# Performance work log

Hardware: AMD Instinct MI355X
Metric: run time of the kernel (lower is better)

Reference implementation:

```python
import jax, jax.numpy as jnp
import numpy as np

N, T, D, M = 16, 4096, 256, 512


def setup_inputs() -> dict:
    key = jax.random.key(0)
    k1, k2 = jax.random.split(key)
    x = jax.random.normal(k1, (N, T, D), dtype=jnp.float32)
    # codebook initialized like the module: uniform(-1/M, 1/M) then row-normalized
    init_bound = 1.0 / M
    emb = jax.random.uniform(k2, (M, D), dtype=jnp.float32, minval=-init_bound, maxval=init_bound)
    emb = emb / (jnp.linalg.norm(emb, axis=1, keepdims=True) + 1e-4)
    return {"x": x, "embedding": emb}


def reference(x, embedding):
    sg = jax.lax.stop_gradient
    # L2_distance: distances computed against the row-normalized codebook,
    # but the gather uses the raw (unnormalized) codebook.
    emb_norm = embedding / (jnp.linalg.norm(embedding, axis=1, keepdims=True) + 1e-4)
    x_flat = sg(x).reshape(-1, D)  # (N*T, D), detached in torch
    distances = (jnp.sum(emb_norm ** 2, axis=1)[None, :]
                 + jnp.sum(x_flat ** 2, axis=1, keepdims=True)
                 - 2.0 * (x_flat @ emb_norm.T))  # (N*T, M)
    indices = jnp.argmin(distances, axis=-1)  # (N*T,)
    encodings = jax.nn.one_hot(indices, M, dtype=jnp.float32)  # (N*T, M)
    quantized = embedding[indices].reshape(x.shape)  # (N, T, D)

    commitment_loss = jnp.mean((sg(x) - quantized) ** 2)
    quantized_ = x + sg(quantized - x)           # straight-through
    quantized_ = (quantized_ + quantized) / 2.0  # averaged with raw-grad path

    avg_probs = jnp.mean(encodings, axis=0)  # (M,)
    perplexity = jnp.exp(-jnp.sum(avg_probs * jnp.log(avg_probs + 1e-10)))
    return quantized_, commitment_loss, perplexity
```

## Files before the change

kernel.cpp:

```cpp
#include <hip/hip_runtime.h>
#include <hip/hip_bf16.h>


typedef _Float16 half8_t __attribute__((ext_vector_type(8)));
typedef _Float16 half4_t __attribute__((ext_vector_type(4)));
typedef float f32x4 __attribute__((ext_vector_type(4)));

static constexpr int kRows = 65536;
static constexpr int kD = 256;
static constexpr int kM = 512;
static constexpr int kBM = 64;

typedef const unsigned int __attribute__((address_space(1)))* gas_t;
typedef unsigned int __attribute__((address_space(3)))* las_t;

__global__ void vq_prep(const float* __restrict__ emb, _Float16* __restrict__ swz,
                        float* __restrict__ bias, unsigned int* __restrict__ hist,
                        float* __restrict__ loss) {
    const int j = blockIdx.x;
    const int lane = threadIdx.x;
    float4 v = ((const float4*)(emb + j * kD))[lane];
    float ss = v.x * v.x + v.y * v.y + v.z * v.z + v.w * v.w;
    #pragma unroll
    for (int off = 32; off > 0; off >>= 1) ss += __shfl_xor(ss, off);
    const float scale = 1.0f / (sqrtf(ss) + 1e-4f);
    if (lane == 0) bias[j] = 0.5f * ss * scale * scale;
    half4_t h;
    h[0] = (_Float16)(v.x * scale);
    h[1] = (_Float16)(v.y * scale);
    h[2] = (_Float16)(v.z * scale);
    h[3] = (_Float16)(v.w * scale);
    const int k0 = lane * 4;
    const int ko = k0 >> 5;
    const int qd = (k0 >> 3) & 3;
    const int jj = k0 & 7;
    const int off_h = (j >> 4) * 4096 + ko * 512 + (qd * 16 + (j & 15)) * 8 + jj;
    *(half4_t*)(swz + off_h) = h;
    if (j == 0) {
        for (int b = lane; b < kM; b += 64) hist[b] = 0u;
        if (lane == 0) loss[0] = 0.0f;
    }
}

__global__ __launch_bounds__(512, 8) void vq_main(
    const float* __restrict__ x, const float* __restrict__ emb,
    const _Float16* __restrict__ bswz, const float* __restrict__ bias,
    unsigned int* __restrict__ hist, float* __restrict__ loss_accum,
    float* __restrict__ out) {
    __shared__ _Float16 bb0[32 * kD];
    __shared__ _Float16 bb1[32 * kD];
    __shared__ float lbias[kM];
    __shared__ unsigned int lhist[kM];
    __shared__ int lidx[kBM];
    __shared__ float lbv[kBM * 2];
    __shared__ int lbi[kBM * 2];
    __shared__ float lred[8];

    const int t = threadIdx.x;
    const int row0 = blockIdx.x * kBM;
    const int wave = t >> 6;
    const int lane = t & 63;
    const int qd = lane >> 4;
    const int ln = lane & 15;
    const int m0 = (wave & 3) * 16;
    const int h = wave >> 2;

    lhist[t] = 0u;
    lbias[t] = bias[t];

    {
        const _Float16* src = bswz + t * 8;
        __builtin_amdgcn_global_load_lds((gas_t)(const void*)(src),
                                         (las_t)(void*)(bb0 + t * 8), 16, 0, 0);
        __builtin_amdgcn_global_load_lds((gas_t)(const void*)(src + 4096),
                                         (las_t)(void*)(bb0 + t * 8 + 4096), 16, 0, 0);
    }

    half8_t a[8];
    {
        const float* xr = x + (size_t)(row0 + m0 + ln) * kD + qd * 8;
        #pragma unroll
        for (int ko = 0; ko < 8; ++ko) {
            const float4 v0 = *(const float4*)(xr + ko * 32);
            const float4 v1 = *(const float4*)(xr + ko * 32 + 4);
            half8_t hh;
            hh[0] = (_Float16)v0.x; hh[1] = (_Float16)v0.y;
            hh[2] = (_Float16)v0.z; hh[3] = (_Float16)v0.w;
            hh[4] = (_Float16)v1.x; hh[5] = (_Float16)v1.y;
            hh[6] = (_Float16)v1.z; hh[7] = (_Float16)v1.w;
            a[ko] = hh;
        }
    }
    __syncthreads();

    float bv[4] = {-1e30f, -1e30f, -1e30f, -1e30f};
    int bi[4] = {0, 0, 0, 0};

    auto issue = [&](int s, _Float16* dst) {
        const _Float16* src = bswz + (size_t)s * 8192 + t * 8;
        __builtin_amdgcn_global_load_lds((gas_t)(const void*)(src),
                                         (las_t)(void*)(dst + t * 8), 16, 0, 0);
        __builtin_amdgcn_global_load_lds((gas_t)(const void*)(src + 4096),
                                         (las_t)(void*)(dst + t * 8 + 4096), 16, 0, 0);
    };
    auto compute = [&](int s, const _Float16* buf) {
        const int c = s * 32 + h * 16 + ln;
        const float bbias = lbias[c];
        f32x4 acc = {-bbias, -bbias, -bbias, -bbias};
        const half8_t* bp = (const half8_t*)buf + h * 512 + lane;
        #pragma unroll
        for (int ko = 0; ko < 8; ++ko)
            acc = __builtin_amdgcn_mfma_f32_16x16x32_f16(a[ko], bp[ko * 64], acc, 0, 0, 0);
        #pragma unroll
        for (int r = 0; r < 4; ++r)
            if (acc[r] > bv[r] || (acc[r] == bv[r] && c < bi[r])) { bv[r] = acc[r]; bi[r] = c; }
    };

    #pragma unroll 1
    for (int s = 0; s < 16; s += 2) {
        issue(s + 1, bb1);
        compute(s, bb0);
        __syncthreads();
        if (s + 2 < 16) issue(s + 2, bb0);
        compute(s + 1, bb1);
        __syncthreads();
    }

    #pragma unroll
    for (int r = 0; r < 4; ++r) {
        #pragma unroll
        for (int off = 1; off < 16; off <<= 1) {
            const float ov = __shfl_xor(bv[r], off);
            const int oi = __shfl_xor(bi[r], off);
            if (ov > bv[r] || (ov == bv[r] && oi < bi[r])) { bv[r] = ov; bi[r] = oi; }
        }
        if (ln == 0) {
            const int row = m0 + qd * 4 + r;
            lbv[row * 2 + h] = bv[r];
            lbi[row * 2 + h] = bi[r];
        }
    }
    __syncthreads();
    if (t < kBM) {
        const float v0 = lbv[t * 2], v1 = lbv[t * 2 + 1];
        const int i0 = lbi[t * 2], i1 = lbi[t * 2 + 1];
        const int win = (v1 > v0 || (v1 == v0 && i1 < i0)) ? i1 : i0;
        lidx[t] = win;
        atomicAdd(&lhist[win], 1u);
    }
    __syncthreads();

    float lsum = 0.0f;
    {
        const float* xg = x + (size_t)row0 * kD;
        float* og = out + (size_t)row0 * kD;
        #pragma unroll
        for (int i = 0; i < 8; ++i) {
            const int g = t * 4 + i * 2048;
            const int r = g >> 8;
            const float4 xv = *(const float4*)(xg + g);
            const int idx = lidx[r];
            const float4 q = *(const float4*)(emb + (size_t)idx * kD + (g & 255));
            const float d0 = xv.x - q.x, d1 = xv.y - q.y, d2 = xv.z - q.z, d3 = xv.w - q.w;
            lsum += d0 * d0 + d1 * d1 + d2 * d2 + d3 * d3;
            float4 o;
            o.x = ((xv.x + (q.x - xv.x)) + q.x) * 0.5f;
            o.y = ((xv.y + (q.y - xv.y)) + q.y) * 0.5f;
            o.z = ((xv.z + (q.z - xv.z)) + q.z) * 0.5f;
            o.w = ((xv.w + (q.w - xv.w)) + q.w) * 0.5f;
            *(float4*)&og[g] = o;
        }
    }
    #pragma unroll
    for (int off = 32; off > 0; off >>= 1) lsum += __shfl_xor(lsum, off);
    if (lane == 0) lred[wave] = lsum;
    __syncthreads();
    if (t == 0) {
        float bs = 0.f;
        #pragma unroll
        for (int w = 0; w < 8; ++w) bs += lred[w];
        atomicAdd(loss_accum, bs);
    }

    const unsigned int h0 = lhist[t];
    if (h0) atomicAdd(&hist[t], h0);
}

__global__ void vq_final(const unsigned int* __restrict__ hist,
                         const float* __restrict__ loss_accum,
                         float* __restrict__ out) {
    const int t = threadIdx.x;
    __shared__ float sr[4];
    float s = 0.0f;
    for (int b = t; b < kM; b += 256) {
        const float p = (float)hist[b] * (1.0f / 65536.0f);
        s += p * logf(p + 1e-10f);
    }
    #pragma unroll
    for (int off = 32; off > 0; off >>= 1) s += __shfl_xor(s, off);
    if ((t & 63) == 0) sr[t >> 6] = s;
    __syncthreads();
    if (t == 0) {
        const float tot = sr[0] + sr[1] + sr[2] + sr[3];
        out[16777217] = expf(-tot);
        out[16777216] = loss_accum[0] * (1.0f / 16777216.0f);
    }
}

extern "C" void kernel_launch(void* const* d_in, const int* in_sizes, int n_in,
                              void* d_out, int out_size, void* d_ws, size_t ws_size,
                              hipStream_t stream) {
    const float* x = (const float*)d_in[0];
    const float* emb = (const float*)d_in[1];
    char* ws = (char*)d_ws;
    _Float16* bswz = (_Float16*)ws;
    float* bias = (float*)(ws + 262144);
    unsigned int* hist = (unsigned int*)(ws + 262144 + 2048);
    float* loss = (float*)(ws + 262144 + 4096);
    float* out = (float*)d_out;

    vq_prep<<<kM, 64, 0, stream>>>(emb, bswz, bias, hist, loss);
    vq_main<<<kRows / kBM, 512, 0, stream>>>(x, emb, bswz, bias, hist, loss, out);
    vq_final<<<1, 256, 0, stream>>>(hist, loss, out);
}
```

Baseline: 144.9 us.

## Compute commitment loss from matmul scores and write codebook rows directly

```diff
diff --git a/kernel.cpp b/kernel.cpp
--- a/kernel.cpp
+++ b/kernel.cpp
@@ -1,5 +1,4 @@
 #include <hip/hip_runtime.h>
-#include <hip/hip_bf16.h>
 
 
 typedef _Float16 half8_t __attribute__((ext_vector_type(8)));
@@ -15,16 +14,21 @@
 typedef unsigned int __attribute__((address_space(3)))* las_t;
 
 __global__ void vq_prep(const float* __restrict__ emb, _Float16* __restrict__ swz,
-                        float* __restrict__ bias, unsigned int* __restrict__ hist,
-                        float* __restrict__ loss) {
+                        float* __restrict__ bias, float2* __restrict__ cab,
+                        unsigned int* __restrict__ hist, float* __restrict__ loss) {
     const int j = blockIdx.x;
     const int lane = threadIdx.x;
     float4 v = ((const float4*)(emb + j * kD))[lane];
     float ss = v.x * v.x + v.y * v.y + v.z * v.z + v.w * v.w;
     #pragma unroll
     for (int off = 32; off > 0; off >>= 1) ss += __shfl_xor(ss, off);
-    const float scale = 1.0f / (sqrtf(ss) + 1e-4f);
-    if (lane == 0) bias[j] = 0.5f * ss * scale * scale;
+    const float s = sqrtf(ss) + 1e-4f;
+    const float scale = 1.0f / s;
+    if (lane == 0) {
+        bias[j] = 0.5f * ss * scale * scale;
+        cab[j] = make_float2(ss * (1.0f - scale),
+                             -2.0f * s);
+    }
     half4_t h;
     h[0] = (_Float16)(v.x * scale);
     h[1] = (_Float16)(v.y * scale);
@@ -42,28 +46,28 @@
     }
 }
 
-__global__ __launch_bounds__(512, 8) void vq_main(
+__global__ __launch_bounds__(512, 4) void vq_main(
     const float* __restrict__ x, const float* __restrict__ emb,
     const _Float16* __restrict__ bswz, const float* __restrict__ bias,
-    unsigned int* __restrict__ hist, float* __restrict__ loss_accum,
-    float* __restrict__ out) {
+    const float2* __restrict__ cab, unsigned int* __restrict__ hist,
+    float* __restrict__ loss_accum, float* __restrict__ out) {
     __shared__ _Float16 bb0[32 * kD];
     __shared__ _Float16 bb1[32 * kD];
     __shared__ float lbias[kM];
     __shared__ unsigned int lhist[kM];
-    __shared__ int lidx[kBM];
-    __shared__ float lbv[kBM * 2];
-    __shared__ int lbi[kBM * 2];
-    __shared__ float lred[8];
+    __shared__ float lbv[kBM][2];
+    __shared__ int   lbi[kBM][2];
+    __shared__ float lssq[kBM];
+    __shared__ int   lidx[kBM];
 
     const int t = threadIdx.x;
-    const int row0 = blockIdx.x * kBM;
     const int wave = t >> 6;
     const int lane = t & 63;
     const int qd = lane >> 4;
     const int ln = lane & 15;
     const int m0 = (wave & 3) * 16;
     const int h = wave >> 2;
+    const int row0 = blockIdx.x * kBM;
 
     lhist[t] = 0u;
     lbias[t] = bias[t];
@@ -77,6 +81,7 @@
     }
 
     half8_t a[8];
+    float ssq = 0.0f;
     {
         const float* xr = x + (size_t)(row0 + m0 + ln) * kD + qd * 8;
         #pragma unroll
@@ -89,8 +94,14 @@
             hh[4] = (_Float16)v1.x; hh[5] = (_Float16)v1.y;
             hh[6] = (_Float16)v1.z; hh[7] = (_Float16)v1.w;
             a[ko] = hh;
-        }
-    }
+            ssq += v0.x*v0.x + v0.y*v0.y + v0.z*v0.z + v0.w*v0.w
+                 + v1.x*v1.x + v1.y*v1.y + v1.z*v1.z + v1.w*v1.w;
+        }
+    }
+    ssq += __shfl_xor(ssq, 16);
+    ssq += __shfl_xor(ssq, 32);
+    if (h == 0 && qd == 0) lssq[m0 + ln] = ssq;
+
     __syncthreads();
 
     float bv[4] = {-1e30f, -1e30f, -1e30f, -1e30f};
@@ -136,54 +147,43 @@
         }
         if (ln == 0) {
             const int row = m0 + qd * 4 + r;
-            lbv[row * 2 + h] = bv[r];
-            lbi[row * 2 + h] = bi[r];
-        }
-    }
-    __syncthreads();
+            lbv[row][h] = bv[r];
+            lbi[row][h] = bi[r];
+        }
+    }
+    __syncthreads();
+
+    float term = 0.0f;
     if (t < kBM) {
-        const float v0 = lbv[t * 2], v1 = lbv[t * 2 + 1];
-        const int i0 = lbi[t * 2], i1 = lbi[t * 2 + 1];
-        const int win = (v1 > v0 || (v1 == v0 && i1 < i0)) ? i1 : i0;
+        const float v0 = lbv[t][0], v1 = lbv[t][1];
+        const int i0 = lbi[t][0], i1 = lbi[t][1];
+        const bool take1 = (v1 > v0);
+        const int win = take1 ? i1 : i0;
+        const float sc = take1 ? v1 : v0;
         lidx[t] = win;
         atomicAdd(&lhist[win], 1u);
-    }
-    __syncthreads();
-
-    float lsum = 0.0f;
+        const float2 cc = cab[win];
+        term = lssq[t] + cc.x + cc.y * sc;
+    }
+    if (wave == 0) {
+        #pragma unroll
+        for (int off = 32; off > 0; off >>= 1) term += __shfl_xor(term, off);
+        if (lane == 0) atomicAdd(loss_accum, term);
+    }
+    __syncthreads();
+
     {
-        const float* xg = x + (size_t)row0 * kD;
-        float* og = out + (size_t)row0 * kD;
-        #pragma unroll
+        float* og = out + (size_t)(row0 + wave * 8) * kD;
+        #pragma unroll 4
         for (int i = 0; i < 8; ++i) {
-            const int g = t * 4 + i * 2048;
-            const int r = g >> 8;
-            const float4 xv = *(const float4*)(xg + g);
-            const int idx = lidx[r];
-            const float4 q = *(const float4*)(emb + (size_t)idx * kD + (g & 255));
-            const float d0 = xv.x - q.x, d1 = xv.y - q.y, d2 = xv.z - q.z, d3 = xv.w - q.w;
-            lsum += d0 * d0 + d1 * d1 + d2 * d2 + d3 * d3;
-            float4 o;
-            o.x = ((xv.x + (q.x - xv.x)) + q.x) * 0.5f;
-            o.y = ((xv.y + (q.y - xv.y)) + q.y) * 0.5f;
-            o.z = ((xv.z + (q.z - xv.z)) + q.z) * 0.5f;
-            o.w = ((xv.w + (q.w - xv.w)) + q.w) * 0.5f;
-            *(float4*)&og[g] = o;
-        }
-    }
-    #pragma unroll
-    for (int off = 32; off > 0; off >>= 1) lsum += __shfl_xor(lsum, off);
-    if (lane == 0) lred[wave] = lsum;
-    __syncthreads();
-    if (t == 0) {
-        float bs = 0.f;
-        #pragma unroll
-        for (int w = 0; w < 8; ++w) bs += lred[w];
-        atomicAdd(loss_accum, bs);
-    }
-
-    const unsigned int h0 = lhist[t];
-    if (h0) atomicAdd(&hist[t], h0);
+            const int idx = lidx[wave * 8 + i];
+            const float4 q = *(const float4*)(emb + (size_t)idx * kD + lane * 4);
+            *(float4*)(og + i * kD + lane * 4) = q;
+        }
+    }
+
+    const unsigned int hv = lhist[t];
+    if (hv) atomicAdd(&hist[t], hv);
 }
 
 __global__ void vq_final(const unsigned int* __restrict__ hist,
@@ -215,11 +215,12 @@
     char* ws = (char*)d_ws;
     _Float16* bswz = (_Float16*)ws;
     float* bias = (float*)(ws + 262144);
-    unsigned int* hist = (unsigned int*)(ws + 262144 + 2048);
-    float* loss = (float*)(ws + 262144 + 4096);
+    unsigned int* hist = (unsigned int*)(ws + 264192);
+    float* loss = (float*)(ws + 266240);
+    float2* cab = (float2*)(ws + 266256);
     float* out = (float*)d_out;
 
-    vq_prep<<<kM, 64, 0, stream>>>(emb, bswz, bias, hist, loss);
-    vq_main<<<kRows / kBM, 512, 0, stream>>>(x, emb, bswz, bias, hist, loss, out);
+    vq_prep<<<kM, 64, 0, stream>>>(emb, bswz, bias, cab, hist, loss);
+    vq_main<<<kRows / kBM, 512, 0, stream>>>(x, emb, bswz, bias, cab, hist, loss, out);
     vq_final<<<1, 256, 0, stream>>>(hist, loss, out);
 }
```

After: 182.9 us. +26.2%, slower.

## Fuse prep, main and final kernels into one cooperative launch

Applied to the files above, without the earlier changes.

```diff
diff --git a/kernel.cpp b/kernel.cpp
--- a/kernel.cpp
+++ b/kernel.cpp
@@ -1,5 +1,7 @@
 #include <hip/hip_runtime.h>
-#include <hip/hip_bf16.h>
+#include <hip/hip_cooperative_groups.h>
+
+namespace cg = cooperative_groups;
 
 
 typedef _Float16 half8_t __attribute__((ext_vector_type(8)));
@@ -13,6 +15,214 @@
 
 typedef const unsigned int __attribute__((address_space(1)))* gas_t;
 typedef unsigned int __attribute__((address_space(3)))* las_t;
+
+__device__ __forceinline__ void vq_main_body(
+    const int blk,
+    const float* __restrict__ x, const float* __restrict__ emb,
+    const _Float16* __restrict__ bswz, const float* __restrict__ bias,
+    unsigned int* __restrict__ hist, float* __restrict__ loss_accum,
+    float* __restrict__ out) {
+    __shared__ _Float16 bb0[32 * kD];
+    __shared__ _Float16 bb1[32 * kD];
+    __shared__ float lbias[kM];
+    __shared__ unsigned int lhist[kM];
+    __shared__ int lidx[kBM];
+    __shared__ float lbv[kBM * 2];
+    __shared__ int lbi[kBM * 2];
+    __shared__ float lred[8];
+
+    const int t = threadIdx.x;
+    const int wave = t >> 6;
+    const int lane = t & 63;
+    const int qd = lane >> 4;
+    const int ln = lane & 15;
+    const int m0 = (wave & 3) * 16;
+    const int h = wave >> 2;
+    const int row0 = blk * kBM;
+
+    lhist[t] = 0u;
+    lbias[t] = bias[t];
+
+    {
+        const _Float16* src = bswz + t * 8;
+        __builtin_amdgcn_global_load_lds((gas_t)(const void*)(src),
+                                         (las_t)(void*)(bb0 + t * 8), 16, 0, 0);
+        __builtin_amdgcn_global_load_lds((gas_t)(const void*)(src + 4096),
+                                         (las_t)(void*)(bb0 + t * 8 + 4096), 16, 0, 0);
+    }
+
+    half8_t a[8];
+    {
+        const float* xr = x + (size_t)(row0 + m0 + ln) * kD + qd * 8;
+        #pragma unroll
+        for (int ko = 0; ko < 8; ++ko) {
+            const float4 v0 = *(const float4*)(xr + ko * 32);
+            const float4 v1 = *(const float4*)(xr + ko * 32 + 4);
+            half8_t hh;
+            hh[0] = (_Float16)v0.x; hh[1] = (_Float16)v0.y;
+            hh[2] = (_Float16)v0.z; hh[3] = (_Float16)v0.w;
+            hh[4] = (_Float16)v1.x; hh[5] = (_Float16)v1.y;
+            hh[6] = (_Float16)v1.z; hh[7] = (_Float16)v1.w;
+            a[ko] = hh;
+        }
+    }
+    __syncthreads();
+
+    float bv[4] = {-1e30f, -1e30f, -1e30f, -1e30f};
+    int bi[4] = {0, 0, 0, 0};
+
+    auto issue = [&](int s, _Float16* dst) {
+        const _Float16* src = bswz + (size_t)s * 8192 + t * 8;
+        __builtin_amdgcn_global_load_lds((gas_t)(const void*)(src),
+                                         (las_t)(void*)(dst + t * 8), 16, 0, 0);
+        __builtin_amdgcn_global_load_lds((gas_t)(const void*)(src + 4096),
+                                         (las_t)(void*)(dst + t * 8 + 4096), 16, 0, 0);
+    };
+    auto compute = [&](int s, const _Float16* buf) {
+        const int c = s * 32 + h * 16 + ln;
+        const float bbias = lbias[c];
+        f32x4 acc = {-bbias, -bbias, -bbias, -bbias};
+        const half8_t* bp = (const half8_t*)buf + h * 512 + lane;
+        #pragma unroll
+        for (int ko = 0; ko < 8; ++ko)
+            acc = __builtin_amdgcn_mfma_f32_16x16x32_f16(a[ko], bp[ko * 64], acc, 0, 0, 0);
+        #pragma unroll
+        for (int r = 0; r < 4; ++r)
+            if (acc[r] > bv[r] || (acc[r] == bv[r] && c < bi[r])) { bv[r] = acc[r]; bi[r] = c; }
+    };
+
+    #pragma unroll 1
+    for (int s = 0; s < 16; s += 2) {
+        issue(s + 1, bb1);
+        compute(s, bb0);
+        __syncthreads();
+        if (s + 2 < 16) issue(s + 2, bb0);
+        compute(s + 1, bb1);
+        __syncthreads();
+    }
+
+    #pragma unroll
+    for (int r = 0; r < 4; ++r) {
+        #pragma unroll
+        for (int off = 1; off < 16; off <<= 1) {
+            const float ov = __shfl_xor(bv[r], off);
+            const int oi = __shfl_xor(bi[r], off);
+            if (ov > bv[r] || (ov == bv[r] && oi < bi[r])) { bv[r] = ov; bi[r] = oi; }
+        }
+        if (ln == 0) {
+            const int row = m0 + qd * 4 + r;
+            lbv[row * 2 + h] = bv[r];
+            lbi[row * 2 + h] = bi[r];
+        }
+    }
+    __syncthreads();
+    if (t < kBM) {
+        const float v0 = lbv[t * 2], v1 = lbv[t * 2 + 1];
+        const int i0 = lbi[t * 2], i1 = lbi[t * 2 + 1];
+        const int win = (v1 > v0 || (v1 == v0 && i1 < i0)) ? i1 : i0;
+        lidx[t] = win;
+        atomicAdd(&lhist[win], 1u);
+    }
+    __syncthreads();
+
+    float lsum = 0.0f;
+    {
+        const float* xg = x + (size_t)row0 * kD;
+        float* og = out + (size_t)row0 * kD;
+        #pragma unroll
+        for (int i = 0; i < 8; ++i) {
+            const int g = t * 4 + i * 2048;
+            const int r = g >> 8;
+            const float4 xv = *(const float4*)(xg + g);
+            const int idx = lidx[r];
+            const float4 q = *(const float4*)(emb + (size_t)idx * kD + (g & 255));
+            const float d0 = xv.x - q.x, d1 = xv.y - q.y, d2 = xv.z - q.z, d3 = xv.w - q.w;
+            lsum += d0 * d0 + d1 * d1 + d2 * d2 + d3 * d3;
+            float4 o;
+            o.x = ((xv.x + (q.x - xv.x)) + q.x) * 0.5f;
+            o.y = ((xv.y + (q.y - xv.y)) + q.y) * 0.5f;
+            o.z = ((xv.z + (q.z - xv.z)) + q.z) * 0.5f;
+            o.w = ((xv.w + (q.w - xv.w)) + q.w) * 0.5f;
+            *(float4*)&og[g] = o;
+        }
+    }
+    #pragma unroll
+    for (int off = 32; off > 0; off >>= 1) lsum += __shfl_xor(lsum, off);
+    if (lane == 0) lred[wave] = lsum;
+    __syncthreads();
+    if (t == 0) {
+        float bs = 0.f;
+        #pragma unroll
+        for (int w = 0; w < 8; ++w) bs += lred[w];
+        atomicAdd(loss_accum, bs);
+    }
+
+    const unsigned int h0 = lhist[t];
+    if (h0) atomicAdd(&hist[t], h0);
+}
+
+__global__ __launch_bounds__(512, 8) void vq_fused(
+    const float* __restrict__ x, const float* __restrict__ emb,
+    _Float16* __restrict__ bswz, float* __restrict__ bias,
+    unsigned int* __restrict__ hist, float* __restrict__ loss_accum,
+    unsigned int* __restrict__ cnt, float* __restrict__ out) {
+    __shared__ float fred[8];
+    __shared__ unsigned int lrank;
+
+    const int t = threadIdx.x;
+    const int wave = t >> 6;
+    const int lane = t & 63;
+    const int blk = blockIdx.x;
+
+    if (blk < 64) {
+        const int j = blk * 8 + wave;
+        float4 v = ((const float4*)(emb + j * kD))[lane];
+        float ss = v.x * v.x + v.y * v.y + v.z * v.z + v.w * v.w;
+        #pragma unroll
+        for (int off = 32; off > 0; off >>= 1) ss += __shfl_xor(ss, off);
+        const float scale = 1.0f / (sqrtf(ss) + 1e-4f);
+        if (lane == 0) bias[j] = 0.5f * ss * scale * scale;
+        half4_t hh;
+        hh[0] = (_Float16)(v.x * scale);
+        hh[1] = (_Float16)(v.y * scale);
+        hh[2] = (_Float16)(v.z * scale);
+        hh[3] = (_Float16)(v.w * scale);
+        const int k0 = lane * 4;
+        const int ko = k0 >> 5;
+        const int qdp = (k0 >> 3) & 3;
+        const int jj = k0 & 7;
+        const int off_h = (j >> 4) * 4096 + ko * 512 + (qdp * 16 + (j & 15)) * 8 + jj;
+        *(half4_t*)(bswz + off_h) = hh;
+    } else if (blk == 64) {
+        atomicExch(&hist[t], 0u);
+        if (t == 0) { atomicExch(loss_accum, 0.0f); atomicExch(cnt, 0u); }
+    }
+    cg::this_grid().sync();
+
+    vq_main_body(blk, x, emb, bswz, bias, hist, loss_accum, out);
+
+    asm volatile("s_waitcnt vmcnt(0)" ::: "memory");
+    __syncthreads();
+    if (t == 0) lrank = atomicAdd(cnt, 1u);
+    __syncthreads();
+    if (lrank == (unsigned int)(gridDim.x - 1)) {
+        const unsigned int hv = atomicAdd(&hist[t], 0u);
+        const float p = (float)hv * (1.0f / 65536.0f);
+        float s = p * logf(p + 1e-10f);
+        #pragma unroll
+        for (int off = 32; off > 0; off >>= 1) s += __shfl_xor(s, off);
+        if (lane == 0) fred[wave] = s;
+        __syncthreads();
+        if (t == 0) {
+            float tot = 0.0f;
+            #pragma unroll
+            for (int w = 0; w < 8; ++w) tot += fred[w];
+            const float lt = atomicAdd(loss_accum, 0.0f);
+            out[16777217] = expf(-tot);
+            out[16777216] = lt * (1.0f / 16777216.0f);
+        }
+    }
+}
 
 __global__ void vq_prep(const float* __restrict__ emb, _Float16* __restrict__ swz,
                         float* __restrict__ bias, unsigned int* __restrict__ hist,
@@ -42,148 +252,12 @@
     }
 }
 
-__global__ __launch_bounds__(512, 8) void vq_main(
+__global__ __launch_bounds__(512, 8) void vq_main_fb(
     const float* __restrict__ x, const float* __restrict__ emb,
     const _Float16* __restrict__ bswz, const float* __restrict__ bias,
     unsigned int* __restrict__ hist, float* __restrict__ loss_accum,
     float* __restrict__ out) {
-    __shared__ _Float16 bb0[32 * kD];
-    __shared__ _Float16 bb1[32 * kD];
-    __shared__ float lbias[kM];
-    __shared__ unsigned int lhist[kM];
-    __shared__ int lidx[kBM];
-    __shared__ float lbv[kBM * 2];
-    __shared__ int lbi[kBM * 2];
-    __shared__ float lred[8];
-
-    const int t = threadIdx.x;
-    const int row0 = blockIdx.x * kBM;
-    const int wave = t >> 6;
-    const int lane = t & 63;
-    const int qd = lane >> 4;
-    const int ln = lane & 15;
-    const int m0 = (wave & 3) * 16;
-    const int h = wave >> 2;
-
-    lhist[t] = 0u;
-    lbias[t] = bias[t];
-
-    {
-        const _Float16* src = bswz + t * 8;
-        __builtin_amdgcn_global_load_lds((gas_t)(const void*)(src),
-                                         (las_t)(void*)(bb0 + t * 8), 16, 0, 0);
-        __builtin_amdgcn_global_load_lds((gas_t)(const void*)(src + 4096),
-                                         (las_t)(void*)(bb0 + t * 8 + 4096), 16, 0, 0);
-    }
-
-    half8_t a[8];
-    {
-        const float* xr = x + (size_t)(row0 + m0 + ln) * kD + qd * 8;
-        #pragma unroll
-        for (int ko = 0; ko < 8; ++ko) {
-            const float4 v0 = *(const float4*)(xr + ko * 32);
-            const float4 v1 = *(const float4*)(xr + ko * 32 + 4);
-            half8_t hh;
-            hh[0] = (_Float16)v0.x; hh[1] = (_Float16)v0.y;
-            hh[2] = (_Float16)v0.z; hh[3] = (_Float16)v0.w;
-            hh[4] = (_Float16)v1.x; hh[5] = (_Float16)v1.y;
-            hh[6] = (_Float16)v1.z; hh[7] = (_Float16)v1.w;
-            a[ko] = hh;
-        }
-    }
-    __syncthreads();
-
-    float bv[4] = {-1e30f, -1e30f, -1e30f, -1e30f};
-    int bi[4] = {0, 0, 0, 0};
-
-    auto issue = [&](int s, _Float16* dst) {
-        const _Float16* src = bswz + (size_t)s * 8192 + t * 8;
-        __builtin_amdgcn_global_load_lds((gas_t)(const void*)(src),
-                                         (las_t)(void*)(dst + t * 8), 16, 0, 0);
-        __builtin_amdgcn_global_load_lds((gas_t)(const void*)(src + 4096),
-                                         (las_t)(void*)(dst + t * 8 + 4096), 16, 0, 0);
-    };
-    auto compute = [&](int s, const _Float16* buf) {
-        const int c = s * 32 + h * 16 + ln;
-        const float bbias = lbias[c];
-        f32x4 acc = {-bbias, -bbias, -bbias, -bbias};
-        const half8_t* bp = (const half8_t*)buf + h * 512 + lane;
-        #pragma unroll
-        for (int ko = 0; ko < 8; ++ko)
-            acc = __builtin_amdgcn_mfma_f32_16x16x32_f16(a[ko], bp[ko * 64], acc, 0, 0, 0);
-        #pragma unroll
-        for (int r = 0; r < 4; ++r)
-            if (acc[r] > bv[r] || (acc[r] == bv[r] && c < bi[r])) { bv[r] = acc[r]; bi[r] = c; }
-    };
-
-    #pragma unroll 1
-    for (int s = 0; s < 16; s += 2) {
-        issue(s + 1, bb1);
-        compute(s, bb0);
-        __syncthreads();
-        if (s + 2 < 16) issue(s + 2, bb0);
-        compute(s + 1, bb1);
-        __syncthreads();
-    }
-
-    #pragma unroll
-    for (int r = 0; r < 4; ++r) {
-        #pragma unroll
-        for (int off = 1; off < 16; off <<= 1) {
-            const float ov = __shfl_xor(bv[r], off);
-            const int oi = __shfl_xor(bi[r], off);
-            if (ov > bv[r] || (ov == bv[r] && oi < bi[r])) { bv[r] = ov; bi[r] = oi; }
-        }
-        if (ln == 0) {
-            const int row = m0 + qd * 4 + r;
-            lbv[row * 2 + h] = bv[r];
-            lbi[row * 2 + h] = bi[r];
-        }
-    }
-    __syncthreads();
-    if (t < kBM) {
-        const float v0 = lbv[t * 2], v1 = lbv[t * 2 + 1];
-        const int i0 = lbi[t * 2], i1 = lbi[t * 2 + 1];
-        const int win = (v1 > v0 || (v1 == v0 && i1 < i0)) ? i1 : i0;
-        lidx[t] = win;
-        atomicAdd(&lhist[win], 1u);
-    }
-    __syncthreads();
-
-    float lsum = 0.0f;
-    {
-        const float* xg = x + (size_t)row0 * kD;
-        float* og = out + (size_t)row0 * kD;
-        #pragma unroll
-        for (int i = 0; i < 8; ++i) {
-            const int g = t * 4 + i * 2048;
-            const int r = g >> 8;
-            const float4 xv = *(const float4*)(xg + g);
-            const int idx = lidx[r];
-            const float4 q = *(const float4*)(emb + (size_t)idx * kD + (g & 255));
-            const float d0 = xv.x - q.x, d1 = xv.y - q.y, d2 = xv.z - q.z, d3 = xv.w - q.w;
-            lsum += d0 * d0 + d1 * d1 + d2 * d2 + d3 * d3;
-            float4 o;
-            o.x = ((xv.x + (q.x - xv.x)) + q.x) * 0.5f;
-            o.y = ((xv.y + (q.y - xv.y)) + q.y) * 0.5f;
-            o.z = ((xv.z + (q.z - xv.z)) + q.z) * 0.5f;
-            o.w = ((xv.w + (q.w - xv.w)) + q.w) * 0.5f;
-            *(float4*)&og[g] = o;
-        }
-    }
-    #pragma unroll
-    for (int off = 32; off > 0; off >>= 1) lsum += __shfl_xor(lsum, off);
-    if (lane == 0) lred[wave] = lsum;
-    __syncthreads();
-    if (t == 0) {
-        float bs = 0.f;
-        #pragma unroll
-        for (int w = 0; w < 8; ++w) bs += lred[w];
-        atomicAdd(loss_accum, bs);
-    }
-
-    const unsigned int h0 = lhist[t];
-    if (h0) atomicAdd(&hist[t], h0);
+    vq_main_body(blockIdx.x, x, emb, bswz, bias, hist, loss_accum, out);
 }
 
 __global__ void vq_final(const unsigned int* __restrict__ hist,
@@ -215,11 +289,19 @@
     char* ws = (char*)d_ws;
     _Float16* bswz = (_Float16*)ws;
     float* bias = (float*)(ws + 262144);
-    unsigned int* hist = (unsigned int*)(ws + 262144 + 2048);
-    float* loss = (float*)(ws + 262144 + 4096);
+    unsigned int* hist = (unsigned int*)(ws + 264192);
+    float* loss = (float*)(ws + 266240);
+    unsigned int* cnt = (unsigned int*)(ws + 266256);
     float* out = (float*)d_out;
 
-    vq_prep<<<kM, 64, 0, stream>>>(emb, bswz, bias, hist, loss);
-    vq_main<<<kRows / kBM, 512, 0, stream>>>(x, emb, bswz, bias, hist, loss, out);
-    vq_final<<<1, 256, 0, stream>>>(hist, loss, out);
-}
+    void* args[] = {(void*)&x, (void*)&emb, (void*)&bswz, (void*)&bias,
+                    (void*)&hist, (void*)&loss, (void*)&cnt, (void*)&out};
+    const hipError_t err = hipLaunchCooperativeKernel(
+        (const void*)vq_fused, dim3(kRows / kBM), dim3(512), args, 0, stream);
+    if (err != hipSuccess) {
+        (void)hipGetLastError();
+        vq_prep<<<kM, 64, 0, stream>>>(emb, bswz, bias, hist, loss);
+        vq_main_fb<<<kRows / kBM, 512, 0, stream>>>(x, emb, bswz, bias, hist, loss, out);
+        vq_final<<<1, 256, 0, stream>>>(hist, loss, out);
+    }
+}
```

After: 229.8 us. 1.59x slower.
